# Optimization experiments

Hardware: AMD Instinct MI355X
Metric: run time of the kernel (lower is better)

Reference implementation:

```python
import jax, jax.numpy as jnp
import numpy as np

EPS = 1e-5
NEG_SLOPE = 0.1  # GeoTransformer UnaryBlock uses LeakyReLU(0.1)
GROUPS = 32


def linear(x, W, b):
    # torch nn.Linear convention: W is (out, in)
    return x @ W.T + b


def group_norm(x, gamma, beta, groups=GROUPS):
    # x: (N, C). Torch applies GroupNorm on (1, C, N): stats over (C//g * N) per group.
    N, C = x.shape
    xg = x.T.reshape(groups, -1)            # (g, C//g * N)
    m = xg.mean(axis=1, keepdims=True)
    v = xg.var(axis=1, keepdims=True)
    xn = ((xg - m) / jnp.sqrt(v + EPS)).reshape(C, N).T
    return xn * gamma + beta


def unary_block(x, W, b, gamma, beta):
    return jax.nn.leaky_relu(group_norm(linear(x, W, b), gamma, beta), NEG_SLOPE)


def setup_inputs() -> dict:
    key = jax.random.key(0)
    ks = jax.random.split(key, 24)
    init_dim = 64
    N2, N3, N4, N5 = 131072, 32768, 8192, 2048
    d2, d3, d4, d5 = init_dim * 4, init_dim * 8, init_dim * 16, 2048
    out_dim = 256
    s = lambda k, shp: jax.random.normal(k, shp, dtype=jnp.float32)
    inp = {
        'feats_s2': s(ks[0], (N2, d2)),
        'feats_s3': s(ks[1], (N3, d3)),
        'feats_s4': s(ks[2], (N4, d4)),
        'feats_s5': s(ks[3], (N5, d5)),
        'up1': jax.random.randint(ks[4], (N2,), 0, N3),
        'up2': jax.random.randint(ks[5], (N3,), 0, N4),
        'up3': jax.random.randint(ks[6], (N4,), 0, N5),
        # inproj: Linear(input_dim, init_dim*32)
        'W_in': s(ks[7], (init_dim * 32, d5)) * 0.02,
        'b_in': s(ks[8], (init_dim * 32,)) * 0.02,
        # decoder4: UnaryBlock(init_dim*48, init_dim*16)
        'W4': s(ks[9], (init_dim * 16, init_dim * 48)) * 0.02,
        'b4': s(ks[10], (init_dim * 16,)) * 0.02,
        'g4': jnp.ones((init_dim * 16,), jnp.float32),
        'beta4': jnp.zeros((init_dim * 16,), jnp.float32),
        # decoder3: UnaryBlock(init_dim*24, init_dim*8)
        'W3': s(ks[11], (init_dim * 8, init_dim * 24)) * 0.02,
        'b3': s(ks[12], (init_dim * 8,)) * 0.02,
        'g3': jnp.ones((init_dim * 8,), jnp.float32),
        'beta3': jnp.zeros((init_dim * 8,), jnp.float32),
        # decoder2: LastUnaryBlock(init_dim*12, output_dim) -> plain Linear
        'W2': s(ks[13], (out_dim, init_dim * 12)) * 0.02,
        'b2': s(ks[14], (out_dim,)) * 0.02,
    }
    return inp


def reference(feats_s2, feats_s3, feats_s4, feats_s5, up1, up2, up3,
              W_in, b_in, W4, b4, g4, beta4, W3, b3, g3, beta3, W2, b2):
    x5 = linear(feats_s5, W_in, b_in)                     # (N5, 2048)
    l4 = jnp.concatenate([x5[up3], feats_s4], axis=1)     # gather + concat (N4, 3072)
    l4 = unary_block(l4, W4, b4, g4, beta4)               # (N4, 1024)
    l3 = jnp.concatenate([l4[up2], feats_s3], axis=1)     # (N3, 1536)
    l3 = unary_block(l3, W3, b3, g3, beta3)               # (N3, 512)
    l2 = jnp.concatenate([l3[up1], feats_s2], axis=1)     # (N2, 768)
    return linear(l2, W2, b2)                             # (N2, 256)
```

## Files before the change

### kernel.cpp

```cpp
#include <hip/hip_runtime.h>
#include <cstdint>
#include <cstddef>

#define DEVI __device__ __forceinline__
#define WAITVM0 asm volatile("s_waitcnt vmcnt(0)" ::: "memory")
#define WAITVM4 asm volatile("s_waitcnt vmcnt(4)" ::: "memory")
#define WAITVM8 asm volatile("s_waitcnt vmcnt(8)" ::: "memory")
#define WAITLGKM asm volatile("s_waitcnt lgkmcnt(0)" ::: "memory")
#define SCHEDB __builtin_amdgcn_sched_barrier(0)

typedef __bf16 bf16x8 __attribute__((ext_vector_type(8)));
typedef float f32x4 __attribute__((ext_vector_type(4)));
typedef uint32_t u32x4 __attribute__((ext_vector_type(4)));

DEVI ushort f2bf(float f) {
  union { float f; uint32_t u; } v; v.f = f;
  uint32_t u = v.u;
  return (ushort)((u + 0x7FFFu + ((u >> 16) & 1u)) >> 16);
}
DEVI float bf2f(ushort h) {
  union { uint32_t u; float f; } v; v.u = ((uint32_t)h) << 16;
  return v.f;
}
DEVI float lrelu(float t) { return t > 0.0f ? t : 0.1f * t; }

DEVI u32x4 cvt8(f32x4 a, f32x4 b) {
  u32x4 o;
  o[0] = (uint32_t)f2bf(a[0]) | ((uint32_t)f2bf(a[1]) << 16);
  o[1] = (uint32_t)f2bf(a[2]) | ((uint32_t)f2bf(a[3]) << 16);
  o[2] = (uint32_t)f2bf(b[0]) | ((uint32_t)f2bf(b[1]) << 16);
  o[3] = (uint32_t)f2bf(b[2]) | ((uint32_t)f2bf(b[3]) << 16);
  return o;
}
DEVI u32x4 gn8(u32x4 d, f32x4 g0, f32x4 g1, f32x4 b0, f32x4 b1) {
  float f0 = bf2f((ushort)(d[0] & 0xffffu)), f1 = bf2f((ushort)(d[0] >> 16));
  float f2 = bf2f((ushort)(d[1] & 0xffffu)), f3 = bf2f((ushort)(d[1] >> 16));
  float f4 = bf2f((ushort)(d[2] & 0xffffu)), f5 = bf2f((ushort)(d[2] >> 16));
  float f6 = bf2f((ushort)(d[3] & 0xffffu)), f7 = bf2f((ushort)(d[3] >> 16));
  float t0 = lrelu(f0 * g0[0] + b0[0]), t1 = lrelu(f1 * g0[1] + b0[1]);
  float t2 = lrelu(f2 * g0[2] + b0[2]), t3 = lrelu(f3 * g0[3] + b0[3]);
  float t4 = lrelu(f4 * g1[0] + b1[0]), t5 = lrelu(f5 * g1[1] + b1[1]);
  float t6 = lrelu(f6 * g1[2] + b1[2]), t7 = lrelu(f7 * g1[3] + b1[3]);
  u32x4 o;
  o[0] = (uint32_t)f2bf(t0) | ((uint32_t)f2bf(t1) << 16);
  o[1] = (uint32_t)f2bf(t2) | ((uint32_t)f2bf(t3) << 16);
  o[2] = (uint32_t)f2bf(t4) | ((uint32_t)f2bf(t5) << 16);
  o[3] = (uint32_t)f2bf(t6) | ((uint32_t)f2bf(t7) << 16);
  return o;
}

DEVI void async_copy16(const void* g, void* l) {
  __attribute__((address_space(1))) void* gp =
      reinterpret_cast<__attribute__((address_space(1))) void*>(
          reinterpret_cast<uintptr_t>(const_cast<void*>(g)));
  __attribute__((address_space(3))) void* lp =
      reinterpret_cast<__attribute__((address_space(3))) void*>(
          static_cast<uint32_t>(reinterpret_cast<uintptr_t>(l)));
  __builtin_amdgcn_global_load_lds(gp, lp, 16, 0, 0);
}

struct CvtSeg { const f32x4* src; u32x4* dst; };
struct CvtArgs { CvtSeg seg[4]; int start[5]; };

__global__ void cvt_multi(CvtArgs a, int total8) {
  int i = blockIdx.x * blockDim.x + threadIdx.x;
  const int stride = gridDim.x * blockDim.x;
  for (; i < total8; i += stride) {
    int s = 0;
#pragma unroll
    for (int j = 1; j < 4; ++j) s += (i >= a.start[j]);
    const int off = i - a.start[s];
    f32x4 f0 = a.seg[s].src[off * 2];
    f32x4 f1 = a.seg[s].src[off * 2 + 1];
    a.seg[s].dst[off] = cvt8(f0, f1);
  }
}

__global__ void zero_kernel(float* __restrict__ p) { p[threadIdx.x] = 0.0f; }

__global__ void gn_coef(const float* __restrict__ stats, const float* __restrict__ gamma,
                        const float* __restrict__ beta, float* __restrict__ ga,
                        float* __restrict__ be, int C, float invcnt) {
  int ch = blockIdx.x * blockDim.x + threadIdx.x;
  if (ch >= C) return;
  int g = ch / (C >> 5);
  float mean = stats[2 * g] * invcnt;
  float var = stats[2 * g + 1] * invcnt - mean * mean;
  float inv = rsqrtf(var + 1e-5f);
  float gm = gamma[ch] * inv;
  ga[ch] = gm;
  be[ch] = beta[ch] - mean * gm;
}

__global__ void gn_apply(const ushort* __restrict__ x, const float* __restrict__ ga,
                         const float* __restrict__ be, ushort* __restrict__ y,
                         int Nrows, int C) {
  const int tpr = C >> 3;
  const int gtid = blockIdx.x * blockDim.x + threadIdx.x;
  const int c8 = (gtid % tpr) * 8;
  const f32x4 g0 = *(const f32x4*)(ga + c8), g1 = *(const f32x4*)(ga + c8 + 4);
  const f32x4 b0 = *(const f32x4*)(be + c8), b1 = *(const f32x4*)(be + c8 + 4);
  const int rstep = (gridDim.x * blockDim.x) / tpr;
  for (int r = gtid / tpr; r < Nrows; r += rstep) {
    u32x4 d = *(const u32x4*)(x + (size_t)r * C + c8);
    *(u32x4*)(y + (size_t)r * C + c8) = gn8(d, g0, g1, b0, b1);
  }
}

template <int EPI, int STATS>
__global__ __launch_bounds__(256, 3) void gemms(
    const ushort* __restrict__ Ag, const float* __restrict__ Adf,
    const int* __restrict__ up, int dg,
    const ushort* __restrict__ Bw, const float* __restrict__ bias,
    void* __restrict__ Cout, float* __restrict__ stats,
    int M, int N, int K) {
  constexpr int BM = 128, BN = 128, BK = 64;
  constexpr int ABY = BM * BK * 2;
  __shared__ __align__(16) char smem[ABY + BN * BK * 2];
  __shared__ int s_up[BM];
  __shared__ float ssum[32], ssq[32];

  const int nbn = N >> 7;
  const int cpx = (int)gridDim.x >> 3;
  const int bid = ((int)blockIdx.x & 7) * cpx + ((int)blockIdx.x >> 3);
  const int bm = bid / nbn, bn = bid % nbn;
  const int row0 = bm * BM, col0 = bn * BN;
  const int tid = threadIdx.x, lane = tid & 63, wave = tid >> 6;
  const int wm = wave >> 1, wn = wave & 1;
  const int dd = K - dg;
  const int ng = dg / BK;
  const int nt = K / BK;

  if (up != nullptr && tid < BM) s_up[tid] = up[row0 + tid];
  if constexpr (STATS) { if (tid < 32) { ssum[tid] = 0.f; ssq[tid] = 0.f; } }
  __syncthreads();

  int cs_[4];
  const ushort* pG[4]; const float* pD[4];
#pragma unroll
  for (int li = 0; li < 4; ++li) {
    const int chunk = li * 256 + tid;
    const int r = chunk >> 3;
    cs_[li] = ((chunk & 7) ^ (r & 7)) << 3;
    pG[li] = (ng > 0) ? (Ag + (size_t)s_up[r] * dg + cs_[li]) : nullptr;
    pD[li] = (ng < nt) ? (Adf + (size_t)(row0 + r) * dd + cs_[li]) : nullptr;
  }
  const ushort* pB[4];
#pragma unroll
  for (int li = 0; li < 4; ++li) {
    const int chunk = li * 256 + tid;
    const int rb = chunk >> 3;
    pB[li] = Bw + (size_t)(col0 + rb) * K + (((chunk & 7) ^ (rb & 7)) << 3);
  }

  f32x4 rdv[8];

  auto issueAg = [&](int t) {
#pragma unroll
    for (int li = 0; li < 4; ++li)
      async_copy16(pG[li] + t * BK, smem + li * 4096 + wave * 1024);
  };
  auto issueB = [&](int t) {
#pragma unroll
    for (int li = 0; li < 4; ++li)
      async_copy16(pB[li] + t * BK, smem + ABY + li * 4096 + wave * 1024);
  };
  auto issueRdv = [&](int t) {
    const int kd = t * BK - dg;
#pragma unroll
    for (int li = 0; li < 4; ++li) {
      rdv[2 * li]     = *(const f32x4*)(pD[li] + kd);
      rdv[2 * li + 1] = *(const f32x4*)(pD[li] + kd + 4);
    }
  };
  auto dsWrite = [&]() {
#pragma unroll
    for (int li = 0; li < 4; ++li)
      *(u32x4*)(smem + li * 4096 + tid * 16) = cvt8(rdv[2 * li], rdv[2 * li + 1]);
  };

  int offA[2][4], offB[2][4];
#pragma unroll
  for (int kk = 0; kk < 2; ++kk) {
    const int ch = kk * 4 + (lane >> 4);
#pragma unroll
    for (int m = 0; m < 4; ++m) {
      const int ra = wm * 64 + m * 16 + (lane & 15);
      offA[kk][m] = ra * 128 + ((ch ^ (ra & 7)) << 4);
    }
#pragma unroll
    for (int n = 0; n < 4; ++n) {
      const int rb = wn * 64 + n * 16 + (lane & 15);
      offB[kk][n] = ABY + rb * 128 + ((ch ^ (rb & 7)) << 4);
    }
  }

  if (ng == 0) issueRdv(0);

  f32x4 acc[4][4] = {};
  for (int t = 0; t < nt; ++t) {
    const bool curD = (t >= ng);
    const bool nxtDirect = (t + 1 < nt) && (t + 1 >= ng);
    if (!curD) issueAg(t);
    issueB(t);
    if (curD) {
      WAITVM4;
      SCHEDB;
      dsWrite();
    }
    if (nxtDirect) issueRdv(t + 1);
    if (nxtDirect) { WAITVM8; } else { WAITVM0; }
    WAITLGKM;
    SCHEDB;
    __builtin_amdgcn_s_barrier();
#pragma unroll
    for (int kk = 0; kk < 2; ++kk) {
      bf16x8 af[4], bv[4];
#pragma unroll
      for (int m = 0; m < 4; ++m) af[m] = *(const bf16x8*)(smem + offA[kk][m]);
#pragma unroll
      for (int n = 0; n < 4; ++n) bv[n] = *(const bf16x8*)(smem + offB[kk][n]);
      __builtin_amdgcn_s_setprio(1);
#pragma unroll
      for (int m = 0; m < 4; ++m)
#pragma unroll
        for (int n = 0; n < 4; ++n)
          acc[m][n] = __builtin_amdgcn_mfma_f32_16x16x32_bf16(af[m], bv[n], acc[m][n], 0, 0, 0);
      __builtin_amdgcn_s_setprio(0);
    }
    __builtin_amdgcn_s_barrier();
  }

  const int cr = (lane >> 4) << 2;
  const int cc = lane & 15;
  float sacc[4] = {0, 0, 0, 0}, qacc[4] = {0, 0, 0, 0};
#pragma unroll
  for (int n = 0; n < 4; ++n) {
    const int colg = col0 + wn * 64 + n * 16 + cc;
    const float bvv = bias[colg];
#pragma unroll
    for (int m = 0; m < 4; ++m) {
      const int rowg = row0 + wm * 64 + m * 16 + cr;
#pragma unroll
      for (int r2 = 0; r2 < 4; ++r2) {
        const float v = acc[m][n][r2] + bvv;
        if constexpr (STATS) { sacc[n] += v; qacc[n] += v * v; }
        if constexpr (EPI == 0)
          ((ushort*)Cout)[(size_t)(rowg + r2) * N + colg] = f2bf(v);
        else
          ((float*)Cout)[(size_t)(rowg + r2) * N + colg] = v;
      }
    }
  }
  if constexpr (STATS) {
    const int gsize = N >> 5;
#pragma unroll
    for (int n = 0; n < 4; ++n) {
      float s = sacc[n], q = qacc[n];
      s += __shfl_xor(s, 16); q += __shfl_xor(q, 16);
      s += __shfl_xor(s, 32); q += __shfl_xor(q, 32);
      if (lane < 16) {
        const int colg = col0 + wn * 64 + n * 16 + lane;
        const int g = colg / gsize;
        atomicAdd(&ssum[g], s);
        atomicAdd(&ssq[g], q);
      }
    }
    __syncthreads();
    if (tid < 32) {
      const int g0 = col0 / gsize, g1 = (col0 + BN) / gsize;
      if (tid >= g0 && tid < g1) {
        atomicAdd(&stats[2 * tid], ssum[tid]);
        atomicAdd(&stats[2 * tid + 1], ssq[tid]);
      }
    }
  }
}

extern "C" void kernel_launch(void* const* d_in, const int* in_sizes, int n_in,
                              void* d_out, int out_size, void* d_ws, size_t ws_size,
                              hipStream_t stream) {
  const float* s2   = (const float*)d_in[0];
  const float* s3   = (const float*)d_in[1];
  const float* s4   = (const float*)d_in[2];
  const float* s5   = (const float*)d_in[3];
  const int*   up1  = (const int*)d_in[4];
  const int*   up2  = (const int*)d_in[5];
  const int*   up3  = (const int*)d_in[6];
  const float* W_in = (const float*)d_in[7];
  const float* b_in = (const float*)d_in[8];
  const float* W4   = (const float*)d_in[9];
  const float* b4   = (const float*)d_in[10];
  const float* g4   = (const float*)d_in[11];
  const float* bt4  = (const float*)d_in[12];
  const float* W3   = (const float*)d_in[13];
  const float* b3   = (const float*)d_in[14];
  const float* g3   = (const float*)d_in[15];
  const float* bt3  = (const float*)d_in[16];
  const float* W2   = (const float*)d_in[17];
  const float* b2   = (const float*)d_in[18];
  float* out = (float*)d_out;
  char* ws = (char*)d_ws;

  ushort* Winb  = (ushort*)(ws + 0);
  ushort* W4b   = (ushort*)(ws + 8388608);
  ushort* W3b   = (ushort*)(ws + 14680064);
  ushort* W2b   = (ushort*)(ws + 16252928);
  float*  stats = (float*)(ws + 16646144);
  float*  cga4  = (float*)(ws + 16646656);
  float*  cbe4  = (float*)(ws + 16650752);
  float*  cga3  = (float*)(ws + 16654848);
  float*  cbe3  = (float*)(ws + 16656896);
  ushort* x5b   = (ushort*)(ws + 16777216);
  ushort* l4lin = (ushort*)(ws + 25165824);
  ushort* l4b   = (ushort*)(ws + 41943040);
  ushort* l3lin = (ushort*)(ws + 58720256);
  ushort* l3b   = (ushort*)(ws + 92274688);

  zero_kernel<<<1, 128, 0, stream>>>(stats);

  CvtArgs ca;
  const float* srcs[4] = { W_in, W4, W3, W2 };
  ushort* dsts[4] = { Winb, W4b, W3b, W2b };
  long ns[4] = { 2048L*2048, 1024L*3072, 512L*1536, 256L*768 };
  int cum = 0;
  for (int i = 0; i < 4; ++i) {
    ca.seg[i].src = (const f32x4*)srcs[i];
    ca.seg[i].dst = (u32x4*)dsts[i];
    ca.start[i] = cum;
    cum += (int)(ns[i] >> 3);
  }
  ca.start[4] = cum;
  cvt_multi<<<1024, 256, 0, stream>>>(ca, cum);

  gemms<0, 0><<<256, 256, 0, stream>>>(
      nullptr, s5, nullptr, 0, Winb, b_in, x5b, nullptr, 2048, 2048, 2048);
  gemms<0, 1><<<512, 256, 0, stream>>>(
      x5b, s4, up3, 2048, W4b, b4, l4lin, stats, 8192, 1024, 3072);
  gn_coef<<<4, 256, 0, stream>>>(stats, g4, bt4, cga4, cbe4, 1024, 1.0f / 262144.0f);
  gn_apply<<<2048, 256, 0, stream>>>(l4lin, cga4, cbe4, l4b, 8192, 1024);
  gemms<0, 1><<<1024, 256, 0, stream>>>(
      l4b, s3, up2, 1024, W3b, b3, l3lin, stats + 64, 32768, 512, 1536);
  gn_coef<<<2, 256, 0, stream>>>(stats + 64, g3, bt3, cga3, cbe3, 512, 1.0f / 524288.0f);
  gn_apply<<<2048, 256, 0, stream>>>(l3lin, cga3, cbe3, l3b, 32768, 512);
  gemms<1, 0><<<2048, 256, 0, stream>>>(
      l3b, s2, up1, 512, W2b, b2, out, nullptr, 131072, 256, 768);

  (void)in_sizes; (void)n_in; (void)out_size; (void)ws_size;
}
```

Baseline: 323.8 us.

## Double-buffer LDS tiles in GEMM to overlap loads with MFMA

Converts the single-buffered GEMM main loop into a two-stage LDS ping-pong. Tile t+2 (async gather/weights, or fp32 direct loads converted and written to the other buffer) is issued while MFMAs consume the current buffer. The goal is to hide global memory latency that the old load-then-compute loop exposed. In exchange LDS use doubles to 64KB per block and launch bounds drop from 3 to 2 blocks per CU, which lowers occupancy.

```diff
diff --git a/kernel.cpp b/kernel.cpp
--- a/kernel.cpp
+++ b/kernel.cpp
@@ -108,7 +108,7 @@
 }
 
 template <int EPI, int STATS>
-__global__ __launch_bounds__(256, 3) void gemms(
+__global__ __launch_bounds__(256, 2) void gemmq(
     const ushort* __restrict__ Ag, const float* __restrict__ Adf,
     const int* __restrict__ up, int dg,
     const ushort* __restrict__ Bw, const float* __restrict__ bias,
@@ -116,7 +116,8 @@
     int M, int N, int K) {
   constexpr int BM = 128, BN = 128, BK = 64;
   constexpr int ABY = BM * BK * 2;
-  __shared__ __align__(16) char smem[ABY + BN * BK * 2];
+  constexpr int BUF = ABY + BN * BK * 2;
+  __shared__ __align__(16) char smem[2 * BUF];
   __shared__ int s_up[BM];
   __shared__ float ssum[32], ssq[32];
 
@@ -155,28 +156,29 @@
 
   f32x4 rdv[8];
 
-  auto issueAg = [&](int t) {
+  auto issueA = [&](int t, char* buf) {
+    if (t < ng) {
+#pragma unroll
+      for (int li = 0; li < 4; ++li)
+        async_copy16(pG[li] + t * BK, buf + li * 4096 + wave * 1024);
+    } else {
+      const int kd = t * BK - dg;
+#pragma unroll
+      for (int li = 0; li < 4; ++li) {
+        rdv[2 * li]     = *(const f32x4*)(pD[li] + kd);
+        rdv[2 * li + 1] = *(const f32x4*)(pD[li] + kd + 4);
+      }
+    }
+  };
+  auto issueB = [&](int t, char* buf) {
 #pragma unroll
     for (int li = 0; li < 4; ++li)
-      async_copy16(pG[li] + t * BK, smem + li * 4096 + wave * 1024);
+      async_copy16(pB[li] + t * BK, buf + ABY + li * 4096 + wave * 1024);
   };
-  auto issueB = [&](int t) {
+  auto dsWrite = [&](char* buf) {
 #pragma unroll
     for (int li = 0; li < 4; ++li)
-      async_copy16(pB[li] + t * BK, smem + ABY + li * 4096 + wave * 1024);
-  };
-  auto issueRdv = [&](int t) {
-    const int kd = t * BK - dg;
-#pragma unroll
-    for (int li = 0; li < 4; ++li) {
-      rdv[2 * li]     = *(const f32x4*)(pD[li] + kd);
-      rdv[2 * li + 1] = *(const f32x4*)(pD[li] + kd + 4);
-    }
-  };
-  auto dsWrite = [&]() {
-#pragma unroll
-    for (int li = 0; li < 4; ++li)
-      *(u32x4*)(smem + li * 4096 + tid * 16) = cvt8(rdv[2 * li], rdv[2 * li + 1]);
+      *(u32x4*)(buf + li * 4096 + tid * 16) = cvt8(rdv[2 * li], rdv[2 * li + 1]);
   };
 
   int offA[2][4], offB[2][4];
@@ -195,40 +197,56 @@
     }
   }
 
-  if (ng == 0) issueRdv(0);
+  issueA(0, smem);
+  issueB(0, smem);
+  if (ng == 0) {
+    WAITVM4;
+    SCHEDB;
+    dsWrite(smem);
+  }
+  issueA(1, smem + BUF);
+  issueB(1, smem + BUF);
+  WAITVM8;
+  WAITLGKM;
+  SCHEDB;
+  __builtin_amdgcn_s_barrier();
 
   f32x4 acc[4][4] = {};
+  int c = 0;
   for (int t = 0; t < nt; ++t) {
-    const bool curD = (t >= ng);
-    const bool nxtDirect = (t + 1 < nt) && (t + 1 >= ng);
-    if (!curD) issueAg(t);
-    issueB(t);
-    if (curD) {
+    char* bufc = smem + c * BUF;
+    char* bufo = smem + (c ^ 1) * BUF;
+    if (t + 1 < nt && t + 1 >= ng) {
       WAITVM4;
       SCHEDB;
-      dsWrite();
-    }
-    if (nxtDirect) issueRdv(t + 1);
-    if (nxtDirect) { WAITVM8; } else { WAITVM0; }
+      dsWrite(bufo);
+    }
+#pragma unroll
+    for (int kk = 0; kk < 2; ++kk) {
+      bf16x8 af[4], bv[4];
+#pragma unroll
+      for (int m = 0; m < 4; ++m) af[m] = *(const bf16x8*)(bufc + offA[kk][m]);
+#pragma unroll
+      for (int n = 0; n < 4; ++n) bv[n] = *(const bf16x8*)(bufc + offB[kk][n]);
+      __builtin_amdgcn_s_setprio(1);
+#pragma unroll
+      for (int m = 0; m < 4; ++m)
+#pragma unroll
+        for (int n = 0; n < 4; ++n)
+          acc[m][n] = __builtin_amdgcn_mfma_f32_16x16x32_bf16(af[m], bv[n], acc[m][n], 0, 0, 0);
+      __builtin_amdgcn_s_setprio(0);
+    }
+    if (t + 1 >= nt) break;
+    __builtin_amdgcn_s_barrier();
+    if (t + 2 < nt) {
+      issueA(t + 2, bufc);
+      issueB(t + 2, bufc);
+    }
+    if (t + 2 < nt) { WAITVM8; } else { WAITVM0; }
     WAITLGKM;
     SCHEDB;
     __builtin_amdgcn_s_barrier();
-#pragma unroll
-    for (int kk = 0; kk < 2; ++kk) {
-      bf16x8 af[4], bv[4];
-#pragma unroll
-      for (int m = 0; m < 4; ++m) af[m] = *(const bf16x8*)(smem + offA[kk][m]);
-#pragma unroll
-      for (int n = 0; n < 4; ++n) bv[n] = *(const bf16x8*)(smem + offB[kk][n]);
-      __builtin_amdgcn_s_setprio(1);
-#pragma unroll
-      for (int m = 0; m < 4; ++m)
-#pragma unroll
-        for (int n = 0; n < 4; ++n)
-          acc[m][n] = __builtin_amdgcn_mfma_f32_16x16x32_bf16(af[m], bv[n], acc[m][n], 0, 0, 0);
-      __builtin_amdgcn_s_setprio(0);
-    }
-    __builtin_amdgcn_s_barrier();
+    c ^= 1;
   }
 
   const int cr = (lane >> 4) << 2;
@@ -333,17 +351,17 @@
   ca.start[4] = cum;
   cvt_multi<<<1024, 256, 0, stream>>>(ca, cum);
 
-  gemms<0, 0><<<256, 256, 0, stream>>>(
+  gemmq<0, 0><<<256, 256, 0, stream>>>(
       nullptr, s5, nullptr, 0, Winb, b_in, x5b, nullptr, 2048, 2048, 2048);
-  gemms<0, 1><<<512, 256, 0, stream>>>(
+  gemmq<0, 1><<<512, 256, 0, stream>>>(
       x5b, s4, up3, 2048, W4b, b4, l4lin, stats, 8192, 1024, 3072);
   gn_coef<<<4, 256, 0, stream>>>(stats, g4, bt4, cga4, cbe4, 1024, 1.0f / 262144.0f);
   gn_apply<<<2048, 256, 0, stream>>>(l4lin, cga4, cbe4, l4b, 8192, 1024);
-  gemms<0, 1><<<1024, 256, 0, stream>>>(
+  gemmq<0, 1><<<1024, 256, 0, stream>>>(
       l4b, s3, up2, 1024, W3b, b3, l3lin, stats + 64, 32768, 512, 1536);
   gn_coef<<<2, 256, 0, stream>>>(stats + 64, g3, bt3, cga3, cbe3, 512, 1.0f / 524288.0f);
   gn_apply<<<2048, 256, 0, stream>>>(l3lin, cga3, cbe3, l3b, 32768, 512);
-  gemms<1, 0><<<2048, 256, 0, stream>>>(
+  gemmq<1, 0><<<2048, 256, 0, stream>>>(
       l3b, s2, up1, 512, W2b, b2, out, nullptr, 131072, 256, 768);
 
   (void)in_sizes; (void)n_in; (void)out_size; (void)ws_size;
```

Measured after the change: 381.4 us. +17.8%, slower.

## Add 512-thread 128x256 tile GEMM variant for decoder layers

Applied to the files above, without the earlier changes.

Adds a new gemmw kernel using 8 waves per block and a wider 128x256 output tile, and switches the three decoder GEMMs (the gather+concat layers) to it, halving block counts. The wider N tile increases reuse of the gathered/converted A rows so each A row is loaded and converted to bf16 fewer times. The trade-offs are more LDS per block (48KB) and a launch bound of 3 blocks per CU, which may cut occupancy. For the last layer (N=256) one block now covers all columns, so A is read once.

```diff
diff --git a/kernel.cpp b/kernel.cpp
--- a/kernel.cpp
+++ b/kernel.cpp
@@ -210,6 +210,176 @@
     }
     if (nxtDirect) issueRdv(t + 1);
     if (nxtDirect) { WAITVM8; } else { WAITVM0; }
+    WAITLGKM;
+    SCHEDB;
+    __builtin_amdgcn_s_barrier();
+#pragma unroll
+    for (int kk = 0; kk < 2; ++kk) {
+      bf16x8 af[4], bv[4];
+#pragma unroll
+      for (int m = 0; m < 4; ++m) af[m] = *(const bf16x8*)(smem + offA[kk][m]);
+#pragma unroll
+      for (int n = 0; n < 4; ++n) bv[n] = *(const bf16x8*)(smem + offB[kk][n]);
+      __builtin_amdgcn_s_setprio(1);
+#pragma unroll
+      for (int m = 0; m < 4; ++m)
+#pragma unroll
+        for (int n = 0; n < 4; ++n)
+          acc[m][n] = __builtin_amdgcn_mfma_f32_16x16x32_bf16(af[m], bv[n], acc[m][n], 0, 0, 0);
+      __builtin_amdgcn_s_setprio(0);
+    }
+    __builtin_amdgcn_s_barrier();
+  }
+
+  const int cr = (lane >> 4) << 2;
+  const int cc = lane & 15;
+  float sacc[4] = {0, 0, 0, 0}, qacc[4] = {0, 0, 0, 0};
+#pragma unroll
+  for (int n = 0; n < 4; ++n) {
+    const int colg = col0 + wn * 64 + n * 16 + cc;
+    const float bvv = bias[colg];
+#pragma unroll
+    for (int m = 0; m < 4; ++m) {
+      const int rowg = row0 + wm * 64 + m * 16 + cr;
+#pragma unroll
+      for (int r2 = 0; r2 < 4; ++r2) {
+        const float v = acc[m][n][r2] + bvv;
+        if constexpr (STATS) { sacc[n] += v; qacc[n] += v * v; }
+        if constexpr (EPI == 0)
+          ((ushort*)Cout)[(size_t)(rowg + r2) * N + colg] = f2bf(v);
+        else
+          ((float*)Cout)[(size_t)(rowg + r2) * N + colg] = v;
+      }
+    }
+  }
+  if constexpr (STATS) {
+    const int gsize = N >> 5;
+#pragma unroll
+    for (int n = 0; n < 4; ++n) {
+      float s = sacc[n], q = qacc[n];
+      s += __shfl_xor(s, 16); q += __shfl_xor(q, 16);
+      s += __shfl_xor(s, 32); q += __shfl_xor(q, 32);
+      if (lane < 16) {
+        const int colg = col0 + wn * 64 + n * 16 + lane;
+        const int g = colg / gsize;
+        atomicAdd(&ssum[g], s);
+        atomicAdd(&ssq[g], q);
+      }
+    }
+    __syncthreads();
+    if (tid < 32) {
+      const int g0 = col0 / gsize, g1 = (col0 + BN) / gsize;
+      if (tid >= g0 && tid < g1) {
+        atomicAdd(&stats[2 * tid], ssum[tid]);
+        atomicAdd(&stats[2 * tid + 1], ssq[tid]);
+      }
+    }
+  }
+}
+
+template <int EPI, int STATS>
+__global__ __launch_bounds__(512, 3) void gemmw(
+    const ushort* __restrict__ Ag, const float* __restrict__ Adf,
+    const int* __restrict__ up, int dg,
+    const ushort* __restrict__ Bw, const float* __restrict__ bias,
+    void* __restrict__ Cout, float* __restrict__ stats,
+    int M, int N, int K) {
+  constexpr int BM = 128, BN = 256, BK = 64;
+  constexpr int ABY = BM * BK * 2;
+  __shared__ __align__(16) char smem[ABY + BN * BK * 2];
+  __shared__ int s_up[BM];
+  __shared__ float ssum[32], ssq[32];
+
+  const int nbn = N >> 8;
+  const int cpx = (int)gridDim.x >> 3;
+  const int bid = ((int)blockIdx.x & 7) * cpx + ((int)blockIdx.x >> 3);
+  const int bm = bid / nbn, bn = bid % nbn;
+  const int row0 = bm * BM, col0 = bn * BN;
+  const int tid = threadIdx.x, lane = tid & 63, wave = tid >> 6;
+  const int wm = wave >> 2, wn = wave & 3;
+  const int dd = K - dg;
+  const int ng = dg / BK;
+  const int nt = K / BK;
+
+  if (up != nullptr && tid < BM) s_up[tid] = up[row0 + tid];
+  if constexpr (STATS) { if (tid < 32) { ssum[tid] = 0.f; ssq[tid] = 0.f; } }
+  __syncthreads();
+
+  int cs_[2];
+  const ushort* pG[2]; const float* pD[2];
+#pragma unroll
+  for (int li = 0; li < 2; ++li) {
+    const int chunk = li * 512 + tid;
+    const int r = chunk >> 3;
+    cs_[li] = ((chunk & 7) ^ (r & 7)) << 3;
+    pG[li] = (ng > 0) ? (Ag + (size_t)s_up[r] * dg + cs_[li]) : nullptr;
+    pD[li] = (ng < nt) ? (Adf + (size_t)(row0 + r) * dd + cs_[li]) : nullptr;
+  }
+  const ushort* pB[4];
+#pragma unroll
+  for (int li = 0; li < 4; ++li) {
+    const int chunk = li * 512 + tid;
+    const int rb = chunk >> 3;
+    pB[li] = Bw + (size_t)(col0 + rb) * K + (((chunk & 7) ^ (rb & 7)) << 3);
+  }
+
+  f32x4 rdv[4];
+
+  auto issueAg = [&](int t) {
+#pragma unroll
+    for (int li = 0; li < 2; ++li)
+      async_copy16(pG[li] + t * BK, smem + li * 8192 + wave * 1024);
+  };
+  auto issueB = [&](int t) {
+#pragma unroll
+    for (int li = 0; li < 4; ++li)
+      async_copy16(pB[li] + t * BK, smem + ABY + li * 8192 + wave * 1024);
+  };
+  auto issueRdv = [&](int t) {
+    const int kd = t * BK - dg;
+#pragma unroll
+    for (int li = 0; li < 2; ++li) {
+      rdv[2 * li]     = *(const f32x4*)(pD[li] + kd);
+      rdv[2 * li + 1] = *(const f32x4*)(pD[li] + kd + 4);
+    }
+  };
+  auto dsWrite = [&]() {
+#pragma unroll
+    for (int li = 0; li < 2; ++li)
+      *(u32x4*)(smem + li * 8192 + tid * 16) = cvt8(rdv[2 * li], rdv[2 * li + 1]);
+  };
+
+  int offA[2][4], offB[2][4];
+#pragma unroll
+  for (int kk = 0; kk < 2; ++kk) {
+    const int ch = kk * 4 + (lane >> 4);
+#pragma unroll
+    for (int m = 0; m < 4; ++m) {
+      const int ra = wm * 64 + m * 16 + (lane & 15);
+      offA[kk][m] = ra * 128 + ((ch ^ (ra & 7)) << 4);
+    }
+#pragma unroll
+    for (int n = 0; n < 4; ++n) {
+      const int rb = wn * 64 + n * 16 + (lane & 15);
+      offB[kk][n] = ABY + rb * 128 + ((ch ^ (rb & 7)) << 4);
+    }
+  }
+
+  if (ng == 0) issueRdv(0);
+
+  f32x4 acc[4][4] = {};
+  for (int t = 0; t < nt; ++t) {
+    const bool curD = (t >= ng);
+    const bool nxtD = (t + 1 < nt) && (t + 1 >= ng);
+    if (!curD) issueAg(t);
+    issueB(t);
+    if (curD) {
+      WAITVM4;
+      SCHEDB;
+      dsWrite();
+    }
+    if (nxtD) issueRdv(t + 1);
+    if (nxtD) { WAITVM4; } else { WAITVM0; }
     WAITLGKM;
     SCHEDB;
     __builtin_amdgcn_s_barrier();
@@ -335,15 +505,15 @@
 
   gemms<0, 0><<<256, 256, 0, stream>>>(
       nullptr, s5, nullptr, 0, Winb, b_in, x5b, nullptr, 2048, 2048, 2048);
-  gemms<0, 1><<<512, 256, 0, stream>>>(
+  gemmw<0, 1><<<256, 512, 0, stream>>>(
       x5b, s4, up3, 2048, W4b, b4, l4lin, stats, 8192, 1024, 3072);
   gn_coef<<<4, 256, 0, stream>>>(stats, g4, bt4, cga4, cbe4, 1024, 1.0f / 262144.0f);
   gn_apply<<<2048, 256, 0, stream>>>(l4lin, cga4, cbe4, l4b, 8192, 1024);
-  gemms<0, 1><<<1024, 256, 0, stream>>>(
+  gemmw<0, 1><<<512, 512, 0, stream>>>(
       l4b, s3, up2, 1024, W3b, b3, l3lin, stats + 64, 32768, 512, 1536);
   gn_coef<<<2, 256, 0, stream>>>(stats + 64, g3, bt3, cga3, cbe3, 512, 1.0f / 524288.0f);
   gn_apply<<<2048, 256, 0, stream>>>(l3lin, cga3, cbe3, l3b, 32768, 512);
-  gemms<1, 0><<<2048, 256, 0, stream>>>(
+  gemmw<1, 0><<<1024, 512, 0, stream>>>(
       l3b, s2, up1, 512, W2b, b2, out, nullptr, 131072, 256, 768);
 
   (void)in_sizes; (void)n_in; (void)out_size; (void)ws_size;
```

New measurement: 362.5 us. +12.0%, slower.

## Fuse GroupNorm apply and LeakyReLU into the gathered A-operand load of next GEMM

Applied to the files above, without the earlier changes.

Removes the two standalone gn_apply passes and instead applies the per-channel GroupNorm scale/shift and LeakyReLU while staging gathered rows of the previous layer into LDS in the next GEMM. Coefficients are cached in shared memory, and the gathered part now goes through registers rather than async direct-to-LDS copies. This saves a full read and write of l4 and l3 intermediates plus two kernel launches. The cost is extra ALU work and lost async copy overlap for the gathered K range, since gathered rows are re-normalized once per reuse.

```diff
diff --git a/kernel.cpp b/kernel.cpp
--- a/kernel.cpp
+++ b/kernel.cpp
@@ -92,25 +92,11 @@
   be[ch] = beta[ch] - mean * gm;
 }
 
-__global__ void gn_apply(const ushort* __restrict__ x, const float* __restrict__ ga,
-                         const float* __restrict__ be, ushort* __restrict__ y,
-                         int Nrows, int C) {
-  const int tpr = C >> 3;
-  const int gtid = blockIdx.x * blockDim.x + threadIdx.x;
-  const int c8 = (gtid % tpr) * 8;
-  const f32x4 g0 = *(const f32x4*)(ga + c8), g1 = *(const f32x4*)(ga + c8 + 4);
-  const f32x4 b0 = *(const f32x4*)(be + c8), b1 = *(const f32x4*)(be + c8 + 4);
-  const int rstep = (gridDim.x * blockDim.x) / tpr;
-  for (int r = gtid / tpr; r < Nrows; r += rstep) {
-    u32x4 d = *(const u32x4*)(x + (size_t)r * C + c8);
-    *(u32x4*)(y + (size_t)r * C + c8) = gn8(d, g0, g1, b0, b1);
-  }
-}
-
-template <int EPI, int STATS>
+template <int GNG, int EPI, int STATS>
 __global__ __launch_bounds__(256, 3) void gemms(
     const ushort* __restrict__ Ag, const float* __restrict__ Adf,
     const int* __restrict__ up, int dg,
+    const float* __restrict__ gacoef, const float* __restrict__ becoef,
     const ushort* __restrict__ Bw, const float* __restrict__ bias,
     void* __restrict__ Cout, float* __restrict__ stats,
     int M, int N, int K) {
@@ -119,6 +105,8 @@
   __shared__ __align__(16) char smem[ABY + BN * BK * 2];
   __shared__ int s_up[BM];
   __shared__ float ssum[32], ssq[32];
+  __shared__ float sga[GNG ? 1024 : 4];
+  __shared__ float sbe[GNG ? 1024 : 4];
 
   const int nbn = N >> 7;
   const int cpx = (int)gridDim.x >> 3;
@@ -133,6 +121,12 @@
 
   if (up != nullptr && tid < BM) s_up[tid] = up[row0 + tid];
   if constexpr (STATS) { if (tid < 32) { ssum[tid] = 0.f; ssq[tid] = 0.f; } }
+  if constexpr (GNG) {
+    for (int i = tid * 4; i < dg; i += 1024) {
+      *(f32x4*)&sga[i] = *(const f32x4*)(gacoef + i);
+      *(f32x4*)&sbe[i] = *(const f32x4*)(becoef + i);
+    }
+  }
   __syncthreads();
 
   int cs_[4];
@@ -153,8 +147,14 @@
     pB[li] = Bw + (size_t)(col0 + rb) * K + (((chunk & 7) ^ (rb & 7)) << 3);
   }
 
+  u32x4 rg[4];
   f32x4 rdv[8];
 
+  auto nreg = [&](int t) -> int {
+    if (t >= nt) return 0;
+    if (t < ng) return GNG ? 4 : 0;
+    return 8;
+  };
   auto issueAg = [&](int t) {
 #pragma unroll
     for (int li = 0; li < 4; ++li)
@@ -165,18 +165,35 @@
     for (int li = 0; li < 4; ++li)
       async_copy16(pB[li] + t * BK, smem + ABY + li * 4096 + wave * 1024);
   };
-  auto issueRdv = [&](int t) {
-    const int kd = t * BK - dg;
-#pragma unroll
-    for (int li = 0; li < 4; ++li) {
-      rdv[2 * li]     = *(const f32x4*)(pD[li] + kd);
-      rdv[2 * li + 1] = *(const f32x4*)(pD[li] + kd + 4);
-    }
-  };
-  auto dsWrite = [&]() {
-#pragma unroll
-    for (int li = 0; li < 4; ++li)
-      *(u32x4*)(smem + li * 4096 + tid * 16) = cvt8(rdv[2 * li], rdv[2 * li + 1]);
+  auto issueReg = [&](int t) {
+    if (GNG && t < ng) {
+      const int k0 = t * BK;
+#pragma unroll
+      for (int li = 0; li < 4; ++li) rg[li] = *(const u32x4*)(pG[li] + k0);
+    } else {
+      const int kd = t * BK - dg;
+#pragma unroll
+      for (int li = 0; li < 4; ++li) {
+        rdv[2 * li]     = *(const f32x4*)(pD[li] + kd);
+        rdv[2 * li + 1] = *(const f32x4*)(pD[li] + kd + 4);
+      }
+    }
+  };
+  auto dsWrite = [&](int t) {
+    if (GNG && t < ng) {
+      const int k0 = t * BK;
+#pragma unroll
+      for (int li = 0; li < 4; ++li) {
+        const int cb = k0 + cs_[li];
+        f32x4 g0 = *(const f32x4*)&sga[cb], g1 = *(const f32x4*)&sga[cb + 4];
+        f32x4 b0 = *(const f32x4*)&sbe[cb], b1 = *(const f32x4*)&sbe[cb + 4];
+        *(u32x4*)(smem + li * 4096 + tid * 16) = gn8(rg[li], g0, g1, b0, b1);
+      }
+    } else {
+#pragma unroll
+      for (int li = 0; li < 4; ++li)
+        *(u32x4*)(smem + li * 4096 + tid * 16) = cvt8(rdv[2 * li], rdv[2 * li + 1]);
+    }
   };
 
   int offA[2][4], offB[2][4];
@@ -195,21 +212,23 @@
     }
   }
 
-  if (ng == 0) issueRdv(0);
+  if (nreg(0)) issueReg(0);
 
   f32x4 acc[4][4] = {};
   for (int t = 0; t < nt; ++t) {
-    const bool curD = (t >= ng);
-    const bool nxtDirect = (t + 1 < nt) && (t + 1 >= ng);
-    if (!curD) issueAg(t);
+    const bool curReg = (t < ng) ? (GNG != 0) : true;
+    if (!curReg) issueAg(t);
     issueB(t);
-    if (curD) {
+    if (curReg) {
       WAITVM4;
       SCHEDB;
-      dsWrite();
-    }
-    if (nxtDirect) issueRdv(t + 1);
-    if (nxtDirect) { WAITVM8; } else { WAITVM0; }
+      dsWrite(t);
+    }
+    const int nr1 = nreg(t + 1);
+    if (nr1) issueReg(t + 1);
+    if (nr1 == 8)      { WAITVM8; }
+    else if (nr1 == 4) { WAITVM4; }
+    else               { WAITVM0; }
     WAITLGKM;
     SCHEDB;
     __builtin_amdgcn_s_barrier();
@@ -313,9 +332,7 @@
   float*  cbe3  = (float*)(ws + 16656896);
   ushort* x5b   = (ushort*)(ws + 16777216);
   ushort* l4lin = (ushort*)(ws + 25165824);
-  ushort* l4b   = (ushort*)(ws + 41943040);
-  ushort* l3lin = (ushort*)(ws + 58720256);
-  ushort* l3b   = (ushort*)(ws + 92274688);
+  ushort* l3lin = (ushort*)(ws + 41943040);
 
   zero_kernel<<<1, 128, 0, stream>>>(stats);
 
@@ -333,18 +350,20 @@
   ca.start[4] = cum;
   cvt_multi<<<1024, 256, 0, stream>>>(ca, cum);
 
-  gemms<0, 0><<<256, 256, 0, stream>>>(
-      nullptr, s5, nullptr, 0, Winb, b_in, x5b, nullptr, 2048, 2048, 2048);
-  gemms<0, 1><<<512, 256, 0, stream>>>(
-      x5b, s4, up3, 2048, W4b, b4, l4lin, stats, 8192, 1024, 3072);
+  gemms<0, 0, 0><<<256, 256, 0, stream>>>(
+      nullptr, s5, nullptr, 0, nullptr, nullptr, Winb, b_in,
+      x5b, nullptr, 2048, 2048, 2048);
+  gemms<0, 0, 1><<<512, 256, 0, stream>>>(
+      x5b, s4, up3, 2048, nullptr, nullptr, W4b, b4,
+      l4lin, stats, 8192, 1024, 3072);
   gn_coef<<<4, 256, 0, stream>>>(stats, g4, bt4, cga4, cbe4, 1024, 1.0f / 262144.0f);
-  gn_apply<<<2048, 256, 0, stream>>>(l4lin, cga4, cbe4, l4b, 8192, 1024);
-  gemms<0, 1><<<1024, 256, 0, stream>>>(
-      l4b, s3, up2, 1024, W3b, b3, l3lin, stats + 64, 32768, 512, 1536);
+  gemms<1, 0, 1><<<1024, 256, 0, stream>>>(
+      l4lin, s3, up2, 1024, cga4, cbe4, W3b, b3,
+      l3lin, stats + 64, 32768, 512, 1536);
   gn_coef<<<2, 256, 0, stream>>>(stats + 64, g3, bt3, cga3, cbe3, 512, 1.0f / 524288.0f);
-  gn_apply<<<2048, 256, 0, stream>>>(l3lin, cga3, cbe3, l3b, 32768, 512);
-  gemms<1, 0><<<2048, 256, 0, stream>>>(
-      l3b, s2, up1, 512, W2b, b2, out, nullptr, 131072, 256, 768);
+  gemms<1, 1, 0><<<2048, 256, 0, stream>>>(
+      l3lin, s2, up1, 512, cga3, cbe3, W2b, b2,
+      out, nullptr, 131072, 256, 768);
 
   (void)in_sizes; (void)n_in; (void)out_size; (void)ws_size;
 }
```

Measured after the change: 492.6 us. 1.52x slower.
